# Kernel optimization log

Hardware: AMD Instinct MI355X
Metric: run time of the kernel (lower is better)

Reference implementation:

```python
import jax, jax.numpy as jnp
import numpy as np

N = 50000       # original graph nodes (= number of subgraphs, one per node)
S = 10          # nodes per subgraph
M = N * S       # combined subgraph nodes
E = 2_000_000   # combined subgraph edges
E0 = 1_000_000  # original edges
NIN, HOP, NOUT, L = 64, 16, 128, 3
D = NIN + HOP   # conv width (80)


def setup_inputs() -> dict:
    key = jax.random.key(0)
    ks = iter(jax.random.split(key, 40))
    rng = np.random.default_rng(0)

    # structured index tensors: subgraph b occupies rows [b*S, (b+1)*S); row b*S is the centroid
    sub_batch = np.repeat(np.arange(N, dtype=np.int64), S)
    nodes_mapper = rng.integers(0, N, size=M, dtype=np.int64)
    nodes_mapper[::S] = np.arange(N)           # centroid: mapper == batch id
    hop_indicator = rng.integers(1, 5, size=M).astype(np.int64)
    hop_indicator[::S] = 0                     # centroid is hop 0
    edge_index = rng.integers(0, M, size=(2, E), dtype=np.int64)
    edges_mapper = rng.integers(0, E0, size=E, dtype=np.int64)

    def lin(k, fin, fout):
        return jax.random.normal(k, (fin, fout), jnp.float32) / np.sqrt(fin)

    inp = dict(
        x=jax.random.normal(next(ks), (N, NIN), jnp.float32),
        edge_attr=jax.random.normal(next(ks), (E0, D), jnp.float32),
        hop_table=jax.random.normal(next(ks), (20, HOP), jnp.float32),
        conv_W=jax.random.normal(next(ks), (L, D, D), jnp.float32) / np.sqrt(D),
        bn_g=jnp.ones((L, D), jnp.float32),
        bn_b=jnp.zeros((L, D), jnp.float32),
        oe_W0=lin(next(ks), D, NOUT), oe_b0=jnp.zeros((NOUT,), jnp.float32),
        oe_W1=lin(next(ks), NOUT, NOUT), oe_b1=jnp.zeros((NOUT,), jnp.float32),
        oe_W2=lin(next(ks), NOUT, NOUT), oe_b2=jnp.zeros((NOUT,), jnp.float32),
        st_W0=lin(next(ks), NOUT, NOUT), st_b0=jnp.zeros((NOUT,), jnp.float32),
        st_W1=lin(next(ks), NOUT, NOUT), st_b1=jnp.zeros((NOUT,), jnp.float32),
        st_W2=lin(next(ks), NOUT, NOUT), st_b2=jnp.zeros((NOUT,), jnp.float32),
        ct_W0=lin(next(ks), NOUT, NOUT), ct_b0=jnp.zeros((NOUT,), jnp.float32),
        ct_W1=lin(next(ks), NOUT, NOUT), ct_b1=jnp.zeros((NOUT,), jnp.float32),
        ct_W2=lin(next(ks), NOUT, NOUT), ct_b2=jnp.zeros((NOUT,), jnp.float32),
        gc_W=lin(next(ks), HOP, NOUT), gc_b=jnp.zeros((NOUT,), jnp.float32),
        gs_W=lin(next(ks), HOP, NOUT), gs_b=jnp.zeros((NOUT,), jnp.float32),
        gx_W=lin(next(ks), HOP, NOUT), gx_b=jnp.zeros((NOUT,), jnp.float32),
        nodes_mapper=jnp.asarray(nodes_mapper),
        edge_index=jnp.asarray(edge_index),
        edges_mapper=jnp.asarray(edges_mapper),
        sub_batch=jnp.asarray(sub_batch),
        hop_indicator=jnp.asarray(hop_indicator),
    )
    return inp


def _mlp3(h, W0, b0, W1, b1, W2, b2, final_act):
    h = jax.nn.relu(h @ W0 + b0)
    h = jax.nn.relu(h @ W1 + b1)
    h = h @ W2 + b2
    return jax.nn.relu(h) if final_act else h


def reference(x, edge_attr, hop_table, conv_W, bn_g, bn_b,
              oe_W0, oe_b0, oe_W1, oe_b1, oe_W2, oe_b2,
              st_W0, st_b0, st_W1, st_b1, st_W2, st_b2,
              ct_W0, ct_b0, ct_W1, ct_b1, ct_W2, ct_b2,
              gc_W, gc_b, gs_W, gs_b, gx_W, gx_b,
              nodes_mapper, edge_index, edges_mapper, sub_batch, hop_indicator):
    src, dst = edge_index[0], edge_index[1]
    ea = edge_attr[edges_mapper]                              # [E, D] gather
    hemb = hop_table[hop_indicator + 1]                       # [M, HOP]
    h = jnp.concatenate([x[nodes_mapper], hemb], axis=-1)     # [M, D]

    # GNN: nlayer x (GINE-style conv -> relu -> batchnorm(batch stats) -> residual)
    for l in range(L):
        msg = h[src] + ea                                     # [E, D]
        agg = jax.ops.segment_sum(msg, dst, num_segments=M)   # scatter-add
        h2 = jax.nn.relu(agg @ conv_W[l])
        mu = jnp.mean(h2, axis=0)
        var = jnp.var(h2, axis=0)
        h2 = (h2 - mu) * jax.lax.rsqrt(var + 1e-5) * bn_g[l] + bn_b[l]
        h = h2 + h                                            # residual

    # output encoder MLP (no final activation)
    h = _mlp3(h, oe_W0, oe_b0, oe_W1, oe_b1, oe_W2, oe_b2, False)  # [M, NOUT]

    # three views with sigmoid hop gates
    g_c = jax.nn.sigmoid(hemb @ gc_W + gc_b)
    g_s = jax.nn.sigmoid(hemb @ gs_W + gs_b)
    g_x = jax.nn.sigmoid(hemb @ gx_W + gx_b)

    cm = (nodes_mapper == sub_batch)[:, None]                 # centroid mask (one per subgraph)
    centroid_x = jax.ops.segment_sum(jnp.where(cm, h * g_c, 0.0), sub_batch, num_segments=N)
    subgraph_x = jax.ops.segment_sum(
        _mlp3(h, st_W0, st_b0, st_W1, st_b1, st_W2, st_b2, True) * g_s, sub_batch, num_segments=N)
    context_x = jax.ops.segment_sum(
        _mlp3(h, ct_W0, ct_b0, ct_W1, ct_b1, ct_W2, ct_b2, True) * g_x, nodes_mapper, num_segments=N)

    return centroid_x + subgraph_x + context_x                # embs_combine_mode='add'
```

## Files before the change

kernel.cpp:

```cpp
#include <hip/hip_runtime.h>


typedef __attribute__((ext_vector_type(8))) short bf16x8;
typedef __attribute__((ext_vector_type(4))) float f32x4;

static constexpr int cN = 50000;
static constexpr int cM = 500000;
static constexpr int cE = 2000000;
static constexpr int cTiles = cM / 16;

static constexpr size_t PCONV0 = 0, PCONV1 = 7680, PCONV2 = 15360, POE0 = 23040,
                        POE1 = 35328, POE2 = 51712, PST0 = 68096, PST1 = 84480,
                        PST2 = 100864, PCT0 = 117248, PCT1 = 133632, PCT2 = 150016;
static constexpr size_t PACK_BYTES = 166400 * 2 + 256;

__device__ __forceinline__ float b2f(unsigned short u) {
  union { unsigned int u; float f; } v; v.u = ((unsigned int)u) << 16; return v.f;
}
__device__ __forceinline__ unsigned short f2b(float f) {
  union { float f; unsigned int u; } v; v.f = f;
  unsigned int x = v.u;
  x += 0x7fffu + ((x >> 16) & 1u);
  return (unsigned short)(x >> 16);
}
__device__ __forceinline__ float sigm(float x) { return 1.0f / (1.0f + __expf(-x)); }
__device__ __forceinline__ f32x4 mfma16(bf16x8 a, bf16x8 b, f32x4 c) {
  return __builtin_amdgcn_mfma_f32_16x16x32_bf16(a, b, c, 0, 0, 0);
}

struct RepackDesc { const float* src; unsigned short* dst; int K; int N; int tiles; };
struct RepackArgs { RepackDesc d[12]; };

__global__ __launch_bounds__(256) void repack_kernel(RepackArgs a) {
  RepackDesc dd = a.d[blockIdx.y];
  int tile = blockIdx.x;
  if (tile >= dd.tiles) return;
  int ncb = dd.N >> 4;
  int c = tile / ncb, cb = tile - c * ncb;
  for (int e = threadIdx.x; e < 512; e += 256) {
    int lane = e >> 3, j = e & 7;
    int k = 32 * c + 8 * (lane >> 4) + j;
    int n = 16 * cb + (lane & 15);
    unsigned short v = (k < dd.K) ? f2b(dd.src[(size_t)k * dd.N + n]) : (unsigned short)0;
    dd.dst[(size_t)tile * 512 + e] = v;
  }
}

__global__ __launch_bounds__(256) void gate_build_kernel(
    const float* __restrict__ ht,
    const float* __restrict__ gsW, const float* __restrict__ gsb,
    const float* __restrict__ gcW, const float* __restrict__ gcb,
    const float* __restrict__ gxW, const float* __restrict__ gxb,
    float* __restrict__ gtab)
{
  int i = blockIdx.x * 256 + threadIdx.x;
  if (i >= 3 * 20 * 128) return;
  int g = i / 2560, rem = i - g * 2560;
  int hi = rem >> 7, col = rem & 127;
  const float* W  = (g == 0) ? gsW : (g == 1) ? gcW : gxW;
  const float* bb = (g == 0) ? gsb : (g == 1) ? gcb : gxb;
  float acc = bb[col];
  #pragma unroll
  for (int k = 0; k < 16; ++k) acc += ht[hi * 16 + k] * W[k * 128 + col];
  gtab[i] = sigm(acc);
}

__global__ __launch_bounds__(256) void build_h_kernel(
    const float* __restrict__ x, const float* __restrict__ ht,
    const int* __restrict__ nmap, const int* __restrict__ hop,
    unsigned short* __restrict__ h)
{
  int i = blockIdx.x * 256 + threadIdx.x;
  if (i >= cM * 20) return;
  int row = i / 20, cc = i - row * 20;
  int col = cc * 4;
  float4 f;
  if (col < 64) {
    f = *(const float4*)(x + (size_t)nmap[row] * 64 + col);
  } else {
    int hi = hop[row] + 1;
    f = *(const float4*)(ht + (size_t)hi * 16 + (col - 64));
  }
  ushort4 o; o.x = f2b(f.x); o.y = f2b(f.y); o.z = f2b(f.z); o.w = f2b(f.w);
  *(ushort4*)(h + (size_t)row * 80 + col) = o;
}

__global__ __launch_bounds__(256) void hist_kernel(const int* __restrict__ ei, int* __restrict__ deg) {
  int e = blockIdx.x * 256 + threadIdx.x;
  if (e < cE) atomicAdd(&deg[ei[cE + e]], 1);
}

__global__ __launch_bounds__(256) void scan1_kernel(const int* __restrict__ deg, int* __restrict__ bsum) {
  __shared__ int s[256];
  int i = blockIdx.x * 256 + threadIdx.x;
  s[threadIdx.x] = (i < cM) ? deg[i] : 0;
  __syncthreads();
  for (int o = 128; o > 0; o >>= 1) {
    if (threadIdx.x < o) s[threadIdx.x] += s[threadIdx.x + o];
    __syncthreads();
  }
  if (threadIdx.x == 0) bsum[blockIdx.x] = s[0];
}

__global__ void scan2_kernel(int* __restrict__ bsum, int nb) {
  if (threadIdx.x == 0 && blockIdx.x == 0) {
    int acc = 0;
    for (int i = 0; i < nb; ++i) { int t = bsum[i]; bsum[i] = acc; acc += t; }
  }
}

__global__ __launch_bounds__(256) void scan3_kernel(
    const int* __restrict__ deg, const int* __restrict__ bsum,
    int* __restrict__ rowptr, int* __restrict__ cursor)
{
  __shared__ int s[256];
  int i = blockIdx.x * 256 + threadIdx.x;
  int v = (i < cM) ? deg[i] : 0;
  s[threadIdx.x] = v;
  __syncthreads();
  for (int o = 1; o < 256; o <<= 1) {
    int t = (threadIdx.x >= o) ? s[threadIdx.x - o] : 0;
    __syncthreads();
    s[threadIdx.x] += t;
    __syncthreads();
  }
  if (i < cM) {
    int ex = bsum[blockIdx.x] + s[threadIdx.x] - v;
    rowptr[i] = ex; cursor[i] = ex;
  }
  if (i == cM - 1) rowptr[cM] = bsum[blockIdx.x] + s[threadIdx.x];
}

__global__ __launch_bounds__(256) void scatter_kernel(
    const int* __restrict__ ei, const int* __restrict__ emap,
    int* __restrict__ cursor, int* __restrict__ srcs, int* __restrict__ em2)
{
  int e = blockIdx.x * 256 + threadIdx.x;
  if (e >= cE) return;
  int d = ei[cE + e];
  int pos = atomicAdd(&cursor[d], 1);
  srcs[pos] = ei[e];
  em2[pos] = emap[e];
}

__global__ __launch_bounds__(320) void eag_rowsum_kernel(
    const float* __restrict__ ea, const int* __restrict__ em2,
    const int* __restrict__ rowptr, unsigned short* __restrict__ eag)
{
  int t = threadIdx.x;
  int r = blockIdx.x * 16 + t / 20;
  int c = (t % 20) * 4;
  if (r >= cM) return;
  int p0 = rowptr[r], p1 = rowptr[r + 1];
  float4 acc = {0.f, 0.f, 0.f, 0.f};
  for (int p = p0; p < p1; ++p) {
    int em = em2[p];
    float4 v = *(const float4*)(ea + (size_t)em * 80 + c);
    acc.x += v.x; acc.y += v.y; acc.z += v.z; acc.w += v.w;
  }
  ushort4 o = {f2b(acc.x), f2b(acc.y), f2b(acc.z), f2b(acc.w)};
  *(ushort4*)(eag + (size_t)r * 80 + c) = o;
}

__global__ __launch_bounds__(320) void aggregate_kernel(
    const unsigned short* __restrict__ h, const unsigned short* __restrict__ eag,
    const int* __restrict__ rowptr, const int* __restrict__ srcs,
    unsigned short* __restrict__ Bo)
{
  int t = threadIdx.x;
  int r = blockIdx.x * 16 + t / 20;
  int c = (t % 20) * 4;
  if (r >= cM) return;
  int p0 = rowptr[r], p1 = rowptr[r + 1];
  ushort4 a0 = *(const ushort4*)(eag + (size_t)r * 80 + c);
  float4 acc = {b2f(a0.x), b2f(a0.y), b2f(a0.z), b2f(a0.w)};
  for (int p = p0; p < p1; ++p) {
    int s = srcs[p];
    ushort4 v = *(const ushort4*)(h + (size_t)s * 80 + c);
    acc.x += b2f(v.x); acc.y += b2f(v.y); acc.z += b2f(v.z); acc.w += b2f(v.w);
  }
  ushort4 o = {f2b(acc.x), f2b(acc.y), f2b(acc.z), f2b(acc.w)};
  *(ushort4*)(Bo + (size_t)r * 80 + c) = o;
}

__global__ __launch_bounds__(256) void edge_scatter_kernel(
    const unsigned short* __restrict__ h, const float* __restrict__ ea,
    const int* __restrict__ ei, const int* __restrict__ emap,
    float* __restrict__ agg)
{
  int i = blockIdx.x * 256 + threadIdx.x;
  if (i >= cE * 20) return;
  int e = i / 20, q = i - e * 20;
  int src = ei[e], dst = ei[cE + e], em = emap[e];
  ushort4 hv = *(const ushort4*)(h + (size_t)src * 80 + q * 4);
  float4 ev = *(const float4*)(ea + (size_t)em * 80 + q * 4);
  float* ap = agg + (size_t)dst * 80 + q * 4;
  atomicAdd(ap + 0, b2f(hv.x) + ev.x);
  atomicAdd(ap + 1, b2f(hv.y) + ev.y);
  atomicAdd(ap + 2, b2f(hv.z) + ev.z);
  atomicAdd(ap + 3, b2f(hv.w) + ev.w);
}

template<bool F32IO>
__global__ __launch_bounds__(256) void conv_gemm_kernel(
    void* __restrict__ aggv, const unsigned short* __restrict__ Bp)
{
  __shared__ __align__(16) unsigned short Bl[7680];
  #pragma unroll
  for (int i = threadIdx.x; i < 960; i += 256)
    ((uint4*)Bl)[i] = ((const uint4*)Bp)[i];
  __syncthreads();
  int lane = threadIdx.x & 63, wave = threadIdx.x >> 6;
  int tile0 = (blockIdx.x * 4 + wave) * 4;
  int quad = lane >> 4, m = lane & 15;

  bf16x8 a[4][3];
  #pragma unroll
  for (int tt = 0; tt < 4; ++tt) {
    int tile = tile0 + tt;
    bool act = tile < cTiles;
    size_t rowA = (size_t)tile * 16 + m;
    #pragma unroll
    for (int c = 0; c < 3; ++c) {
      bf16x8 av = {0, 0, 0, 0, 0, 0, 0, 0};
      int k = 32 * c + 8 * quad;
      if (act && k + 8 <= 80) {
        if constexpr (F32IO) {
          const float* p = (const float*)aggv + rowA * 80 + k;
          float4 f0 = *(const float4*)p;
          float4 f1 = *(const float4*)(p + 4);
          av[0] = (short)f2b(f0.x); av[1] = (short)f2b(f0.y);
          av[2] = (short)f2b(f0.z); av[3] = (short)f2b(f0.w);
          av[4] = (short)f2b(f1.x); av[5] = (short)f2b(f1.y);
          av[6] = (short)f2b(f1.z); av[7] = (short)f2b(f1.w);
        } else {
          av = *(const bf16x8*)((const unsigned short*)aggv + rowA * 80 + k);
        }
      }
      a[tt][c] = av;
    }
  }

  #pragma unroll
  for (int tt = 0; tt < 4; ++tt) {
    int tile = tile0 + tt;
    bool act = tile < cTiles;
    #pragma unroll
    for (int cb = 0; cb < 5; ++cb) {
      f32x4 acc = {0.f, 0.f, 0.f, 0.f};
      #pragma unroll
      for (int c = 0; c < 3; ++c)
        acc = mfma16(a[tt][c], *(const bf16x8*)(Bl + ((size_t)(c * 5 + cb) * 64 + lane) * 8), acc);
      int col = cb * 16 + m;
      #pragma unroll
      for (int i2 = 0; i2 < 4; ++i2) {
        size_t row = (size_t)tile * 16 + quad * 4 + i2;
        if (act) {
          float v = fmaxf(acc[i2], 0.0f);
          if constexpr (F32IO) ((float*)aggv)[row * 80 + col] = v;
          else ((unsigned short*)aggv)[row * 80 + col] = f2b(v);
        }
      }
    }
  }
}

template<bool F32IO>
__global__ __launch_bounds__(256) void stats_kernel(
    const void* __restrict__ h2v, float* __restrict__ stats)
{
  __shared__ __align__(16) float ssum[12 * 80];
  __shared__ __align__(16) float ssq[12 * 80];
  int t = threadIdx.x;
  int cc = t % 20, slot = t / 20;
  if (slot < 12) {
    float s0 = 0, s1 = 0, s2 = 0, s3 = 0, q0 = 0, q1 = 0, q2 = 0, q3 = 0;
    for (int row = blockIdx.x * 12 + slot; row < cM; row += gridDim.x * 12) {
      float f0, f1, f2, f3;
      if constexpr (F32IO) {
        float4 v = *(const float4*)((const float*)h2v + (size_t)row * 80 + cc * 4);
        f0 = v.x; f1 = v.y; f2 = v.z; f3 = v.w;
      } else {
        ushort4 v = *(const ushort4*)((const unsigned short*)h2v + (size_t)row * 80 + cc * 4);
        f0 = b2f(v.x); f1 = b2f(v.y); f2 = b2f(v.z); f3 = b2f(v.w);
      }
      s0 += f0; s1 += f1; s2 += f2; s3 += f3;
      q0 += f0 * f0; q1 += f1 * f1; q2 += f2 * f2; q3 += f3 * f3;
    }
    int base = slot * 80 + cc * 4;
    ssum[base + 0] = s0; ssum[base + 1] = s1; ssum[base + 2] = s2; ssum[base + 3] = s3;
    ssq[base + 0] = q0; ssq[base + 1] = q1; ssq[base + 2] = q2; ssq[base + 3] = q3;
  }
  __syncthreads();
  if (t < 20) {
    for (int j = 0; j < 4; ++j) {
      int c = t * 4 + j;
      float s = 0, q = 0;
      for (int sl = 0; sl < 12; ++sl) { s += ssum[sl * 80 + c]; q += ssq[sl * 80 + c]; }
      atomicAdd(&stats[c], s);
      atomicAdd(&stats[80 + c], q);
    }
  }
}

template<bool F32IO>
__global__ __launch_bounds__(256) void bn_residual_kernel(
    const void* __restrict__ h2v, const float* __restrict__ stats,
    const float* __restrict__ g, const float* __restrict__ b,
    unsigned short* __restrict__ h)
{
  int i = blockIdx.x * 256 + threadIdx.x;
  if (i >= cM * 20) return;
  int row = i / 20, cc = i - row * 20;
  int col = cc * 4;
  float in2[4];
  if constexpr (F32IO) {
    float4 v2 = *(const float4*)((const float*)h2v + (size_t)row * 80 + col);
    in2[0] = v2.x; in2[1] = v2.y; in2[2] = v2.z; in2[3] = v2.w;
  } else {
    ushort4 v2 = *(const ushort4*)((const unsigned short*)h2v + (size_t)row * 80 + col);
    in2[0] = b2f(v2.x); in2[1] = b2f(v2.y); in2[2] = b2f(v2.z); in2[3] = b2f(v2.w);
  }
  ushort4 vh = *(const ushort4*)(h + (size_t)row * 80 + col);
  const float invM = 1.0f / (float)cM;
  unsigned short inh[4] = {vh.x, vh.y, vh.z, vh.w};
  unsigned short o[4];
  #pragma unroll
  for (int j = 0; j < 4; ++j) {
    int c = col + j;
    float mu = stats[c] * invM;
    float var = fmaxf(stats[80 + c] * invM - mu * mu, 0.0f);
    float inv = rsqrtf(var + 1e-5f);
    float val = (in2[j] - mu) * inv * g[c] + b[c] + b2f(inh[j]);
    o[j] = f2b(val);
  }
  ushort4 ov = {o[0], o[1], o[2], o[3]};
  *(ushort4*)(h + (size_t)row * 80 + col) = ov;
}

__device__ __forceinline__ void tb_put(unsigned short* tbw, int row, int col, unsigned short v) {
  int g = (col >> 3) ^ (row & 7);
  tbw[row * 128 + (g << 3) + (col & 7)] = v;
}

__device__ __forceinline__ void tb_to_a(bf16x8* a, const unsigned short* tbw, int lane) {
  int quad = lane >> 4, m = lane & 15;
  #pragma unroll
  for (int c = 0; c < 4; ++c) {
    int sg = ((c << 2) | quad) ^ (m & 7);
    a[c] = *(const bf16x8*)(tbw + m * 128 + (sg << 3));
  }
}

template<int KCH>
__device__ __forceinline__ void layer_relu(
    const bf16x8* a, const unsigned short* Wl, const float* bl,
    unsigned short* tbw, int lane)
{
  int quad = lane >> 4, m = lane & 15;
  #pragma unroll
  for (int cb = 0; cb < 8; ++cb) {
    f32x4 acc = {0.f, 0.f, 0.f, 0.f};
    #pragma unroll
    for (int c = 0; c < KCH; ++c)
      acc = mfma16(a[c], *(const bf16x8*)(Wl + ((size_t)(c * 8 + cb) * 64 + lane) * 8), acc);
    int col = cb * 16 + m;
    float bv = bl[col];
    #pragma unroll
    for (int i2 = 0; i2 < 4; ++i2)
      tb_put(tbw, quad * 4 + i2, col, f2b(fmaxf(acc[i2] + bv, 0.0f)));
  }
}

__device__ __forceinline__ void stageW(unsigned short* Wbuf, const unsigned short* src, int nU4, int t) {
  const uint4* s = (const uint4*)src;
  uint4* d = (uint4*)Wbuf;
  for (int i = t; i < nU4; i += 256) d[i] = s[i];
}

__global__ __launch_bounds__(256, 3) void tail_fused_kernel(
    const unsigned short* __restrict__ h,
    const unsigned short* __restrict__ packs,
    const float* __restrict__ oeb0, const float* __restrict__ oeb1, const float* __restrict__ oeb2,
    const float* __restrict__ stb0, const float* __restrict__ stb1, const float* __restrict__ stb2,
    const float* __restrict__ ctb0, const float* __restrict__ ctb1, const float* __restrict__ ctb2,
    const float* __restrict__ gtab,
    const int* __restrict__ hop, const int* __restrict__ nmap, const int* __restrict__ sb,
    float* __restrict__ outp)
{
  __shared__ __align__(16) unsigned short Wbuf[16384];
  __shared__ __align__(16) unsigned short tb[4][2048];
  __shared__ __align__(16) float biasl[9][128];

  int t = threadIdx.x;
  stageW(Wbuf, packs + POE0, 1536, t);
  if (t < 128) {
    biasl[0][t] = oeb0[t]; biasl[1][t] = oeb1[t]; biasl[2][t] = oeb2[t];
    biasl[3][t] = stb0[t]; biasl[4][t] = stb1[t]; biasl[5][t] = stb2[t];
    biasl[6][t] = ctb0[t]; biasl[7][t] = ctb1[t]; biasl[8][t] = ctb2[t];
  }
  __syncthreads();

  int lane = t & 63, wave = t >> 6;
  int tile = blockIdx.x * 4 + wave;
  bool act = tile < cTiles;
  int quad = lane >> 4, m = lane & 15;
  size_t rowA = (size_t)tile * 16 + m;

  bf16x8 aw[4];
  #pragma unroll
  for (int c = 0; c < 4; ++c) {
    bf16x8 av = {0, 0, 0, 0, 0, 0, 0, 0};
    int k = 32 * c + 8 * quad;
    if (act && c < 3 && k + 8 <= 80)
      av = *(const bf16x8*)(h + rowA * 80 + k);
    aw[c] = av;
  }

  layer_relu<3>(aw, Wbuf, biasl[0], tb[wave], lane);
  tb_to_a(aw, tb[wave], lane);
  __syncthreads();
  stageW(Wbuf, packs + POE1, 2048, t);
  __syncthreads();
  layer_relu<4>(aw, Wbuf, biasl[1], tb[wave], lane);
  tb_to_a(aw, tb[wave], lane);
  __syncthreads();
  stageW(Wbuf, packs + POE2, 2048, t);
  __syncthreads();

  float o_out[8][4];
  bf16x8 a_oe[4];
  {
    #pragma unroll
    for (int cb = 0; cb < 8; ++cb) {
      f32x4 acc = {0.f, 0.f, 0.f, 0.f};
      #pragma unroll
      for (int c = 0; c < 4; ++c)
        acc = mfma16(aw[c], *(const bf16x8*)(Wbuf + ((size_t)(c * 8 + cb) * 64 + lane) * 8), acc);
      int col = cb * 16 + m;
      float bv = biasl[2][col];
      #pragma unroll
      for (int i2 = 0; i2 < 4; ++i2) {
        float val = acc[i2] + bv;
        o_out[cb][i2] = val;
        tb_put(tb[wave], quad * 4 + i2, col, f2b(val));
      }
    }
    tb_to_a(a_oe, tb[wave], lane);
  }
  __syncthreads();
  stageW(Wbuf, packs + PST0, 2048, t);
  __syncthreads();

  layer_relu<4>(a_oe, Wbuf, biasl[3], tb[wave], lane);
  tb_to_a(aw, tb[wave], lane);
  __syncthreads();
  stageW(Wbuf, packs + PST1, 2048, t);
  __syncthreads();
  layer_relu<4>(aw, Wbuf, biasl[4], tb[wave], lane);
  tb_to_a(aw, tb[wave], lane);
  __syncthreads();
  stageW(Wbuf, packs + PST2, 2048, t);
  float* red = (float*)&tb[0][0];
  for (int i = t; i < 1024; i += 256) red[i] = 0.0f;
  int sbBase = sb[blockIdx.x * 64];
  __syncthreads();

  int hi2[4], sbr[4], dstm[4]; bool mk[4];
  #pragma unroll
  for (int i2 = 0; i2 < 4; ++i2) {
    int row = tile * 16 + quad * 4 + i2;
    sbr[i2]  = act ? sb[row] : 0;
    dstm[i2] = act ? nmap[row] : 0;
    mk[i2]   = act && (dstm[i2] == sbr[i2]);
    hi2[i2]  = act ? (hop[row] + 1) : 0;
  }

  #pragma unroll
  for (int cb = 0; cb < 8; ++cb) {
    f32x4 acc = {0.f, 0.f, 0.f, 0.f};
    #pragma unroll
    for (int c = 0; c < 4; ++c)
      acc = mfma16(aw[c], *(const bf16x8*)(Wbuf + ((size_t)(c * 8 + cb) * 64 + lane) * 8), acc);
    int col = cb * 16 + m;
    float bv = biasl[5][col];
    #pragma unroll
    for (int i2 = 0; i2 < 4; ++i2) {
      float v = fmaxf(acc[i2] + bv, 0.0f) * gtab[hi2[i2] * 128 + col];
      if (mk[i2]) v += o_out[cb][i2] * gtab[2560 + hi2[i2] * 128 + col];
      if (act) {
        int slot = sbr[i2] - sbBase;
        if ((unsigned)slot < 8u) atomicAdd(&red[slot * 128 + col], v);
        else atomicAdd(outp + (size_t)sbr[i2] * 128 + col, v);
      }
    }
  }
  __syncthreads();
  for (int i = t; i < 1024; i += 256) {
    float v = red[i];
    if (v != 0.0f)
      atomicAdd(outp + (size_t)(sbBase + (i >> 7)) * 128 + (i & 127), v);
  }
  __syncthreads();
  stageW(Wbuf, packs + PCT0, 2048, t);
  __syncthreads();

  layer_relu<4>(a_oe, Wbuf, biasl[6], tb[wave], lane);
  tb_to_a(aw, tb[wave], lane);
  __syncthreads();
  stageW(Wbuf, packs + PCT1, 2048, t);
  __syncthreads();
  layer_relu<4>(aw, Wbuf, biasl[7], tb[wave], lane);
  tb_to_a(aw, tb[wave], lane);
  __syncthreads();
  stageW(Wbuf, packs + PCT2, 2048, t);
  __syncthreads();

  #pragma unroll
  for (int cb = 0; cb < 8; ++cb) {
    f32x4 acc = {0.f, 0.f, 0.f, 0.f};
    #pragma unroll
    for (int c = 0; c < 4; ++c)
      acc = mfma16(aw[c], *(const bf16x8*)(Wbuf + ((size_t)(c * 8 + cb) * 64 + lane) * 8), acc);
    int col = cb * 16 + m;
    float bv = biasl[8][col];
    #pragma unroll
    for (int i2 = 0; i2 < 4; ++i2) {
      float v = fmaxf(acc[i2] + bv, 0.0f) * gtab[5120 + hi2[i2] * 128 + col];
      if (act) atomicAdd(outp + (size_t)dstm[i2] * 128 + col, v);
    }
  }
}

extern "C" void kernel_launch(void* const* d_in, const int* in_sizes, int n_in,
                              void* d_out, int out_size, void* d_ws, size_t ws_size,
                              hipStream_t stream)
{
  const float* x     = (const float*)d_in[0];
  const float* eattr = (const float*)d_in[1];
  const float* htab  = (const float*)d_in[2];
  const float* convW = (const float*)d_in[3];
  const float* bng   = (const float*)d_in[4];
  const float* bnb   = (const float*)d_in[5];
  const float* oeW0 = (const float*)d_in[6];  const float* oeb0 = (const float*)d_in[7];
  const float* oeW1 = (const float*)d_in[8];  const float* oeb1 = (const float*)d_in[9];
  const float* oeW2 = (const float*)d_in[10]; const float* oeb2 = (const float*)d_in[11];
  const float* stW0 = (const float*)d_in[12]; const float* stb0 = (const float*)d_in[13];
  const float* stW1 = (const float*)d_in[14]; const float* stb1 = (const float*)d_in[15];
  const float* stW2 = (const float*)d_in[16]; const float* stb2 = (const float*)d_in[17];
  const float* ctW0 = (const float*)d_in[18]; const float* ctb0 = (const float*)d_in[19];
  const float* ctW1 = (const float*)d_in[20]; const float* ctb1 = (const float*)d_in[21];
  const float* ctW2 = (const float*)d_in[22]; const float* ctb2 = (const float*)d_in[23];
  const float* gcW = (const float*)d_in[24]; const float* gcb = (const float*)d_in[25];
  const float* gsW = (const float*)d_in[26]; const float* gsb = (const float*)d_in[27];
  const float* gxW = (const float*)d_in[28]; const float* gxb = (const float*)d_in[29];
  const int* nmap = (const int*)d_in[30];
  const int* ei   = (const int*)d_in[31];
  const int* emap = (const int*)d_in[32];
  const int* sb   = (const int*)d_in[33];
  const int* hop  = (const int*)d_in[34];

  if (n_in < 35 ||
      in_sizes[0] != cN * 64 || in_sizes[1] != 1000000 * 80 ||
      in_sizes[2] != 20 * 16 || in_sizes[3] != 3 * 80 * 80 ||
      in_sizes[30] != cM || in_sizes[31] != 2 * cE || in_sizes[32] != cE ||
      in_sizes[33] != cM || in_sizes[34] != cM || out_size != cN * 128)
    return;

  char* ws = (char*)d_ws;
  size_t off = 0;
  auto alloc = [&](size_t bytes) -> void* {
    void* p = ws + off; off += (bytes + 255) & ~(size_t)255; return p;
  };

  unsigned short* h    = (unsigned short*)alloc((size_t)cM * 80 * 2);
  unsigned short* Aeag = (unsigned short*)alloc((size_t)cM * 80 * 2);
  unsigned short* Bagg = (unsigned short*)alloc((size_t)cM * 80 * 2);
  int*   rowptr = (int*)alloc((size_t)(cM + 1) * 4);
  int*   srcs   = (int*)alloc((size_t)cE * 4);
  float* stats  = (float*)alloc(1024);
  float* gtab   = (float*)alloc(3 * 20 * 128 * 4);
  unsigned short* packs = (unsigned short*)alloc(PACK_BYTES);
  size_t needFast = off;
  bool fast = (ws_size >= needFast);

  float* aggF = nullptr;
  if (!fast) {
    off = 0;
    h     = (unsigned short*)alloc((size_t)cM * 80 * 2);
    aggF  = (float*)alloc((size_t)cM * 80 * 4);
    stats = (float*)alloc(1024);
    gtab  = (float*)alloc(3 * 20 * 128 * 4);
    packs = (unsigned short*)alloc(PACK_BYTES);
    if (ws_size < off) return;
  }

  RepackArgs ra;
  auto setd = [&](int idx, const float* src, size_t dstOff, int K, int Nn, int tiles) {
    ra.d[idx].src = src; ra.d[idx].dst = packs + dstOff;
    ra.d[idx].K = K; ra.d[idx].N = Nn; ra.d[idx].tiles = tiles;
  };
  setd(0, convW,          PCONV0, 80, 80, 15);
  setd(1, convW + 6400,   PCONV1, 80, 80, 15);
  setd(2, convW + 12800,  PCONV2, 80, 80, 15);
  setd(3, oeW0, POE0, 80, 128, 24);
  setd(4, oeW1, POE1, 128, 128, 32);
  setd(5, oeW2, POE2, 128, 128, 32);
  setd(6, stW0, PST0, 128, 128, 32);
  setd(7, stW1, PST1, 128, 128, 32);
  setd(8, stW2, PST2, 128, 128, 32);
  setd(9, ctW0, PCT0, 128, 128, 32);
  setd(10, ctW1, PCT1, 128, 128, 32);
  setd(11, ctW2, PCT2, 128, 128, 32);
  repack_kernel<<<dim3(32, 12), 256, 0, stream>>>(ra);
  gate_build_kernel<<<30, 256, 0, stream>>>(htab, gsW, gsb, gcW, gcb, gxW, gxb, gtab);

  const int elemBlocksM = (cM * 20 + 255) / 256;
  const int convBlocks  = (cTiles + 15) / 16;
  const int tailBlocks  = (cTiles + 3) / 4;
  const int rowBlocks   = (cM + 15) / 16;
  const int edgeB256    = (cE + 255) / 256;
  const int scanBlocks  = (cM + 255) / 256;

  build_h_kernel<<<elemBlocksM, 256, 0, stream>>>(x, htab, nmap, hop, h);
  hipMemsetAsync(d_out, 0, (size_t)cN * 128 * 4, stream);

  if (fast) {
    int* deg    = (int*)Bagg;
    int* cursor = deg + cM;
    int* em2    = cursor + cM;
    int* bsum   = em2 + cE;

    hipMemsetAsync(deg, 0, (size_t)cM * 4, stream);
    hist_kernel<<<edgeB256, 256, 0, stream>>>(ei, deg);
    scan1_kernel<<<scanBlocks, 256, 0, stream>>>(deg, bsum);
    scan2_kernel<<<1, 64, 0, stream>>>(bsum, scanBlocks);
    scan3_kernel<<<scanBlocks, 256, 0, stream>>>(deg, bsum, rowptr, cursor);
    scatter_kernel<<<edgeB256, 256, 0, stream>>>(ei, emap, cursor, srcs, em2);
    eag_rowsum_kernel<<<rowBlocks, 320, 0, stream>>>(eattr, em2, rowptr, Aeag);

    for (int l = 0; l < 3; ++l) {
      aggregate_kernel<<<rowBlocks, 320, 0, stream>>>(h, Aeag, rowptr, srcs, Bagg);
      conv_gemm_kernel<false><<<convBlocks, 256, 0, stream>>>(
          Bagg, packs + (l == 0 ? PCONV0 : l == 1 ? PCONV1 : PCONV2));
      hipMemsetAsync(stats, 0, 160 * 4, stream);
      stats_kernel<false><<<1024, 256, 0, stream>>>(Bagg, stats);
      bn_residual_kernel<false><<<elemBlocksM, 256, 0, stream>>>(
          Bagg, stats, bng + l * 80, bnb + l * 80, h);
    }
  } else {
    const int edgeBlocks = (cE * 20) / 256;
    for (int l = 0; l < 3; ++l) {
      hipMemsetAsync(aggF, 0, (size_t)cM * 80 * 4, stream);
      edge_scatter_kernel<<<edgeBlocks, 256, 0, stream>>>(h, eattr, ei, emap, aggF);
      conv_gemm_kernel<true><<<convBlocks, 256, 0, stream>>>(
          aggF, packs + (l == 0 ? PCONV0 : l == 1 ? PCONV1 : PCONV2));
      hipMemsetAsync(stats, 0, 160 * 4, stream);
      stats_kernel<true><<<1024, 256, 0, stream>>>(aggF, stats);
      bn_residual_kernel<true><<<elemBlocksM, 256, 0, stream>>>(
          aggF, stats, bng + l * 80, bnb + l * 80, h);
    }
  }

  tail_fused_kernel<<<tailBlocks, 256, 0, stream>>>(
      h, packs,
      oeb0, oeb1, oeb2, stb0, stb1, stb2, ctb0, ctb1, ctb2,
      gtab, hop, nmap, sb, (float*)d_out);
}
```

Measured before the change: 2.823 ms.

## Fuse aggregation with conv GEMM and prefetch tail MLP weights into registers

Merges the CSR gather-aggregate kernel with the conv GEMM. Each block aggregates 80 rows into shared memory, then runs MFMA on them with the conv weights staged in LDS, which removes one write and one read of the aggregate buffer per layer. In the tail kernel, the next layer's weights are loaded into registers during the current layer's compute and committed to LDS afterwards, replacing synchronous staging. The costs are more register pressure in the tail kernel and extra LDS in the fused kernel, which may lower occupancy.

Result: slower. 3.149 ms (+11.6%).

```diff
diff --git a/kernel.cpp b/kernel.cpp
--- a/kernel.cpp
+++ b/kernel.cpp
@@ -162,25 +162,62 @@
   *(ushort4*)(eag + (size_t)r * 80 + c) = o;
 }
 
-__global__ __launch_bounds__(320) void aggregate_kernel(
+__global__ __launch_bounds__(320) void agg_conv_kernel(
     const unsigned short* __restrict__ h, const unsigned short* __restrict__ eag,
     const int* __restrict__ rowptr, const int* __restrict__ srcs,
-    unsigned short* __restrict__ Bo)
-{
+    const unsigned short* __restrict__ Bp, unsigned short* __restrict__ h2)
+{
+  __shared__ __align__(16) unsigned short Bl[7680];
+  __shared__ __align__(16) unsigned short At[80 * 88];
   int t = threadIdx.x;
-  int r = blockIdx.x * 16 + t / 20;
+  for (int i = t; i < 960; i += 320) ((uint4*)Bl)[i] = ((const uint4*)Bp)[i];
+
+  int rloc = t / 20;
   int c = (t % 20) * 4;
-  if (r >= cM) return;
-  int p0 = rowptr[r], p1 = rowptr[r + 1];
-  ushort4 a0 = *(const ushort4*)(eag + (size_t)r * 80 + c);
-  float4 acc = {b2f(a0.x), b2f(a0.y), b2f(a0.z), b2f(a0.w)};
-  for (int p = p0; p < p1; ++p) {
-    int s = srcs[p];
-    ushort4 v = *(const ushort4*)(h + (size_t)s * 80 + c);
-    acc.x += b2f(v.x); acc.y += b2f(v.y); acc.z += b2f(v.z); acc.w += b2f(v.w);
-  }
-  ushort4 o = {f2b(acc.x), f2b(acc.y), f2b(acc.z), f2b(acc.w)};
-  *(ushort4*)(Bo + (size_t)r * 80 + c) = o;
+  int rowBase = blockIdx.x * 80;
+  #pragma unroll
+  for (int tt = 0; tt < 5; ++tt) {
+    int rl = tt * 16 + rloc;
+    int r = rowBase + rl;
+    ushort4 a0 = *(const ushort4*)(eag + (size_t)r * 80 + c);
+    float4 acc = {b2f(a0.x), b2f(a0.y), b2f(a0.z), b2f(a0.w)};
+    int p0 = rowptr[r], p1 = rowptr[r + 1];
+    for (int p = p0; p < p1; ++p) {
+      int s = srcs[p];
+      ushort4 v = *(const ushort4*)(h + (size_t)s * 80 + c);
+      acc.x += b2f(v.x); acc.y += b2f(v.y); acc.z += b2f(v.z); acc.w += b2f(v.w);
+    }
+    ushort4 o = {f2b(acc.x), f2b(acc.y), f2b(acc.z), f2b(acc.w)};
+    *(ushort4*)(At + (size_t)rl * 88 + c) = o;
+  }
+  __syncthreads();
+
+  int lane = t & 63, wave = t >> 6;
+  int quad = lane >> 4, m = lane & 15;
+  int rl0 = wave * 16;
+  size_t gr0 = (size_t)rowBase + rl0;
+
+  bf16x8 a[3];
+  #pragma unroll
+  for (int cc2 = 0; cc2 < 3; ++cc2) {
+    int k = 32 * cc2 + 8 * quad;
+    bf16x8 av = {0, 0, 0, 0, 0, 0, 0, 0};
+    if (k + 8 <= 80) av = *(const bf16x8*)(At + (size_t)(rl0 + m) * 88 + k);
+    a[cc2] = av;
+  }
+  #pragma unroll
+  for (int cb = 0; cb < 5; ++cb) {
+    f32x4 acc = {0.f, 0.f, 0.f, 0.f};
+    #pragma unroll
+    for (int cc2 = 0; cc2 < 3; ++cc2)
+      acc = mfma16(a[cc2], *(const bf16x8*)(Bl + ((size_t)(cc2 * 5 + cb) * 64 + lane) * 8), acc);
+    int col = cb * 16 + m;
+    #pragma unroll
+    for (int i2 = 0; i2 < 4; ++i2) {
+      size_t row = gr0 + quad * 4 + i2;
+      h2[row * 80 + col] = f2b(fmaxf(acc[i2], 0.0f));
+    }
+  }
 }
 
 __global__ __launch_bounds__(256) void edge_scatter_kernel(
@@ -393,14 +430,6 @@
   __shared__ __align__(16) float biasl[9][128];
 
   int t = threadIdx.x;
-  stageW(Wbuf, packs + POE0, 1536, t);
-  if (t < 128) {
-    biasl[0][t] = oeb0[t]; biasl[1][t] = oeb1[t]; biasl[2][t] = oeb2[t];
-    biasl[3][t] = stb0[t]; biasl[4][t] = stb1[t]; biasl[5][t] = stb2[t];
-    biasl[6][t] = ctb0[t]; biasl[7][t] = ctb1[t]; biasl[8][t] = ctb2[t];
-  }
-  __syncthreads();
-
   int lane = t & 63, wave = t >> 6;
   int tile = blockIdx.x * 4 + wave;
   bool act = tile < cTiles;
@@ -417,15 +446,36 @@
     aw[c] = av;
   }
 
+  stageW(Wbuf, packs + POE0, 1536, t);
+  if (t < 128) {
+    biasl[0][t] = oeb0[t]; biasl[1][t] = oeb1[t]; biasl[2][t] = oeb2[t];
+    biasl[3][t] = stb0[t]; biasl[4][t] = stb1[t]; biasl[5][t] = stb2[t];
+    biasl[6][t] = ctb0[t]; biasl[7][t] = ctb1[t]; biasl[8][t] = ctb2[t];
+  }
+  __syncthreads();
+
+  uint4 wreg[8];
+  auto preload = [&](size_t off) {
+    const uint4* s = (const uint4*)(packs + off);
+    #pragma unroll
+    for (int i = 0; i < 8; ++i) wreg[i] = s[t + i * 256];
+  };
+  auto commit = [&]() {
+    uint4* d = (uint4*)Wbuf;
+    #pragma unroll
+    for (int i = 0; i < 8; ++i) d[t + i * 256] = wreg[i];
+  };
+
+  preload(POE1);
   layer_relu<3>(aw, Wbuf, biasl[0], tb[wave], lane);
   tb_to_a(aw, tb[wave], lane);
   __syncthreads();
-  stageW(Wbuf, packs + POE1, 2048, t);
+  commit(); preload(POE2);
   __syncthreads();
   layer_relu<4>(aw, Wbuf, biasl[1], tb[wave], lane);
   tb_to_a(aw, tb[wave], lane);
   __syncthreads();
-  stageW(Wbuf, packs + POE2, 2048, t);
+  commit(); preload(PST0);
   __syncthreads();
 
   float o_out[8][4];
@@ -449,18 +499,18 @@
     tb_to_a(a_oe, tb[wave], lane);
   }
   __syncthreads();
-  stageW(Wbuf, packs + PST0, 2048, t);
+  commit(); preload(PST1);
   __syncthreads();
 
   layer_relu<4>(a_oe, Wbuf, biasl[3], tb[wave], lane);
   tb_to_a(aw, tb[wave], lane);
   __syncthreads();
-  stageW(Wbuf, packs + PST1, 2048, t);
+  commit(); preload(PST2);
   __syncthreads();
   layer_relu<4>(aw, Wbuf, biasl[4], tb[wave], lane);
   tb_to_a(aw, tb[wave], lane);
   __syncthreads();
-  stageW(Wbuf, packs + PST2, 2048, t);
+  commit(); preload(PCT0);
   float* red = (float*)&tb[0][0];
   for (int i = t; i < 1024; i += 256) red[i] = 0.0f;
   int sbBase = sb[blockIdx.x * 64];
@@ -496,24 +546,23 @@
     }
   }
   __syncthreads();
+  commit(); preload(PCT1);
   for (int i = t; i < 1024; i += 256) {
     float v = red[i];
     if (v != 0.0f)
       atomicAdd(outp + (size_t)(sbBase + (i >> 7)) * 128 + (i & 127), v);
   }
   __syncthreads();
-  stageW(Wbuf, packs + PCT0, 2048, t);
-  __syncthreads();
 
   layer_relu<4>(a_oe, Wbuf, biasl[6], tb[wave], lane);
   tb_to_a(aw, tb[wave], lane);
   __syncthreads();
-  stageW(Wbuf, packs + PCT1, 2048, t);
+  commit(); preload(PCT2);
   __syncthreads();
   layer_relu<4>(aw, Wbuf, biasl[7], tb[wave], lane);
   tb_to_a(aw, tb[wave], lane);
   __syncthreads();
-  stageW(Wbuf, packs + PCT2, 2048, t);
+  commit();
   __syncthreads();
 
   #pragma unroll
@@ -616,8 +665,9 @@
   gate_build_kernel<<<30, 256, 0, stream>>>(htab, gsW, gsb, gcW, gcb, gxW, gxb, gtab);
 
   const int elemBlocksM = (cM * 20 + 255) / 256;
+  const int tailBlocks  = (cTiles + 3) / 4;
+  const int aggcBlocks  = cM / 80;
   const int convBlocks  = (cTiles + 15) / 16;
-  const int tailBlocks  = (cTiles + 3) / 4;
   const int rowBlocks   = (cM + 15) / 16;
   const int edgeB256    = (cE + 255) / 256;
   const int scanBlocks  = (cM + 255) / 256;
@@ -640,9 +690,9 @@
     eag_rowsum_kernel<<<rowBlocks, 320, 0, stream>>>(eattr, em2, rowptr, Aeag);
 
     for (int l = 0; l < 3; ++l) {
-      aggregate_kernel<<<rowBlocks, 320, 0, stream>>>(h, Aeag, rowptr, srcs, Bagg);
-      conv_gemm_kernel<false><<<convBlocks, 256, 0, stream>>>(
-          Bagg, packs + (l == 0 ? PCONV0 : l == 1 ? PCONV1 : PCONV2));
+      agg_conv_kernel<<<aggcBlocks, 320, 0, stream>>>(
+          h, Aeag, rowptr, srcs,
+          packs + (l == 0 ? PCONV0 : l == 1 ? PCONV1 : PCONV2), Bagg);
       hipMemsetAsync(stats, 0, 160 * 4, stream);
       stats_kernel<false><<<1024, 256, 0, stream>>>(Bagg, stats);
       bn_residual_kernel<false><<<elemBlocksM, 256, 0, stream>>>(
```

## Fuse conv GEMM with BN stats and stage CSR indices in LDS

Applied to the files above, without the earlier changes.

Adds a conv_stats kernel that runs the conv GEMM with ReLU, writes bf16 output, and accumulates per-column sum and sum-of-squares through shared-memory atomics then global atomics. This removes the separate stats pass over the aggregated buffer in each of the three layers. The row-gather aggregate and eag kernels now load each block's edge index span into LDS cooperatively before gathering, instead of each thread reading indices from global memory. Risks are atomic contention on the 160 stats floats and LDS fallback overhead when a block's span exceeds 1024.

Result: faster. 2.518 ms (-10.8%).

```diff
diff --git a/kernel.cpp b/kernel.cpp
--- a/kernel.cpp
+++ b/kernel.cpp
@@ -147,16 +147,36 @@
     const float* __restrict__ ea, const int* __restrict__ em2,
     const int* __restrict__ rowptr, unsigned short* __restrict__ eag)
 {
+  __shared__ int s_idx[1024];
+  __shared__ int s_rp[17];
   int t = threadIdx.x;
-  int r = blockIdx.x * 16 + t / 20;
+  int rowBase = blockIdx.x * 16;
+  if (t <= 16) s_rp[t] = rowptr[rowBase + t];
+  __syncthreads();
+  int p0b = s_rp[0];
+  int span = s_rp[16] - p0b;
+  bool lds_ok = (span <= 1024);
+  if (lds_ok)
+    for (int i = t; i < span; i += 320) s_idx[i] = em2[p0b + i];
+  __syncthreads();
+
+  int rl = t / 20;
+  int r = rowBase + rl;
   int c = (t % 20) * 4;
-  if (r >= cM) return;
-  int p0 = rowptr[r], p1 = rowptr[r + 1];
+  int p0 = s_rp[rl], p1 = s_rp[rl + 1];
   float4 acc = {0.f, 0.f, 0.f, 0.f};
-  for (int p = p0; p < p1; ++p) {
-    int em = em2[p];
-    float4 v = *(const float4*)(ea + (size_t)em * 80 + c);
-    acc.x += v.x; acc.y += v.y; acc.z += v.z; acc.w += v.w;
+  if (lds_ok) {
+    for (int p = p0; p < p1; ++p) {
+      int em = s_idx[p - p0b];
+      float4 v = *(const float4*)(ea + (size_t)em * 80 + c);
+      acc.x += v.x; acc.y += v.y; acc.z += v.z; acc.w += v.w;
+    }
+  } else {
+    for (int p = p0; p < p1; ++p) {
+      int em = em2[p];
+      float4 v = *(const float4*)(ea + (size_t)em * 80 + c);
+      acc.x += v.x; acc.y += v.y; acc.z += v.z; acc.w += v.w;
+    }
   }
   ushort4 o = {f2b(acc.x), f2b(acc.y), f2b(acc.z), f2b(acc.w)};
   *(ushort4*)(eag + (size_t)r * 80 + c) = o;
@@ -167,17 +187,37 @@
     const int* __restrict__ rowptr, const int* __restrict__ srcs,
     unsigned short* __restrict__ Bo)
 {
+  __shared__ int s_idx[1024];
+  __shared__ int s_rp[17];
   int t = threadIdx.x;
-  int r = blockIdx.x * 16 + t / 20;
+  int rowBase = blockIdx.x * 16;
+  if (t <= 16) s_rp[t] = rowptr[rowBase + t];
+  __syncthreads();
+  int p0b = s_rp[0];
+  int span = s_rp[16] - p0b;
+  bool lds_ok = (span <= 1024);
+  if (lds_ok)
+    for (int i = t; i < span; i += 320) s_idx[i] = srcs[p0b + i];
+  __syncthreads();
+
+  int rl = t / 20;
+  int r = rowBase + rl;
   int c = (t % 20) * 4;
-  if (r >= cM) return;
-  int p0 = rowptr[r], p1 = rowptr[r + 1];
+  int p0 = s_rp[rl], p1 = s_rp[rl + 1];
   ushort4 a0 = *(const ushort4*)(eag + (size_t)r * 80 + c);
   float4 acc = {b2f(a0.x), b2f(a0.y), b2f(a0.z), b2f(a0.w)};
-  for (int p = p0; p < p1; ++p) {
-    int s = srcs[p];
-    ushort4 v = *(const ushort4*)(h + (size_t)s * 80 + c);
-    acc.x += b2f(v.x); acc.y += b2f(v.y); acc.z += b2f(v.z); acc.w += b2f(v.w);
+  if (lds_ok) {
+    for (int p = p0; p < p1; ++p) {
+      int s = s_idx[p - p0b];
+      ushort4 v = *(const ushort4*)(h + (size_t)s * 80 + c);
+      acc.x += b2f(v.x); acc.y += b2f(v.y); acc.z += b2f(v.z); acc.w += b2f(v.w);
+    }
+  } else {
+    for (int p = p0; p < p1; ++p) {
+      int s = srcs[p];
+      ushort4 v = *(const ushort4*)(h + (size_t)s * 80 + c);
+      acc.x += b2f(v.x); acc.y += b2f(v.y); acc.z += b2f(v.z); acc.w += b2f(v.w);
+    }
   }
   ushort4 o = {f2b(acc.x), f2b(acc.y), f2b(acc.z), f2b(acc.w)};
   *(ushort4*)(Bo + (size_t)r * 80 + c) = o;
@@ -199,6 +239,72 @@
   atomicAdd(ap + 1, b2f(hv.y) + ev.y);
   atomicAdd(ap + 2, b2f(hv.z) + ev.z);
   atomicAdd(ap + 3, b2f(hv.w) + ev.w);
+}
+
+__global__ __launch_bounds__(256) void conv_stats_kernel(
+    unsigned short* __restrict__ agg, const unsigned short* __restrict__ Bp,
+    float* __restrict__ stats)
+{
+  __shared__ __align__(16) unsigned short Bl[7680];
+  __shared__ float s_red[160];
+  int t = threadIdx.x;
+  #pragma unroll
+  for (int i = t; i < 960; i += 256)
+    ((uint4*)Bl)[i] = ((const uint4*)Bp)[i];
+  if (t < 160) s_red[t] = 0.0f;
+  __syncthreads();
+  int lane = t & 63, wave = t >> 6;
+  int tile0 = (blockIdx.x * 4 + wave) * 4;
+  int quad = lane >> 4, m = lane & 15;
+
+  bf16x8 a[4][3];
+  #pragma unroll
+  for (int tt = 0; tt < 4; ++tt) {
+    int tile = tile0 + tt;
+    bool act = tile < cTiles;
+    size_t rowA = (size_t)tile * 16 + m;
+    #pragma unroll
+    for (int c = 0; c < 3; ++c) {
+      bf16x8 av = {0, 0, 0, 0, 0, 0, 0, 0};
+      int k = 32 * c + 8 * quad;
+      if (act && k + 8 <= 80)
+        av = *(const bf16x8*)(agg + rowA * 80 + k);
+      a[tt][c] = av;
+    }
+  }
+
+  float lsum[5] = {0, 0, 0, 0, 0}, lsq[5] = {0, 0, 0, 0, 0};
+  #pragma unroll
+  for (int tt = 0; tt < 4; ++tt) {
+    int tile = tile0 + tt;
+    bool act = tile < cTiles;
+    #pragma unroll
+    for (int cb = 0; cb < 5; ++cb) {
+      f32x4 acc = {0.f, 0.f, 0.f, 0.f};
+      #pragma unroll
+      for (int c = 0; c < 3; ++c)
+        acc = mfma16(a[tt][c], *(const bf16x8*)(Bl + ((size_t)(c * 5 + cb) * 64 + lane) * 8), acc);
+      int col = cb * 16 + m;
+      #pragma unroll
+      for (int i2 = 0; i2 < 4; ++i2) {
+        if (act) {
+          float v = fmaxf(acc[i2], 0.0f);
+          size_t row = (size_t)tile * 16 + quad * 4 + i2;
+          agg[row * 80 + col] = f2b(v);
+          lsum[cb] += v;
+          lsq[cb]  += v * v;
+        }
+      }
+    }
+  }
+  #pragma unroll
+  for (int cb = 0; cb < 5; ++cb) {
+    int col = cb * 16 + m;
+    atomicAdd(&s_red[col], lsum[cb]);
+    atomicAdd(&s_red[80 + col], lsq[cb]);
+  }
+  __syncthreads();
+  if (t < 160) atomicAdd(&stats[t], s_red[t]);
 }
 
 template<bool F32IO>
@@ -616,8 +722,8 @@
   gate_build_kernel<<<30, 256, 0, stream>>>(htab, gsW, gsb, gcW, gcb, gxW, gxb, gtab);
 
   const int elemBlocksM = (cM * 20 + 255) / 256;
+  const int tailBlocks  = (cTiles + 3) / 4;
   const int convBlocks  = (cTiles + 15) / 16;
-  const int tailBlocks  = (cTiles + 3) / 4;
   const int rowBlocks   = (cM + 15) / 16;
   const int edgeB256    = (cE + 255) / 256;
   const int scanBlocks  = (cM + 255) / 256;
@@ -641,10 +747,9 @@
 
     for (int l = 0; l < 3; ++l) {
       aggregate_kernel<<<rowBlocks, 320, 0, stream>>>(h, Aeag, rowptr, srcs, Bagg);
-      conv_gemm_kernel<false><<<convBlocks, 256, 0, stream>>>(
-          Bagg, packs + (l == 0 ? PCONV0 : l == 1 ? PCONV1 : PCONV2));
       hipMemsetAsync(stats, 0, 160 * 4, stream);
-      stats_kernel<false><<<1024, 256, 0, stream>>>(Bagg, stats);
+      conv_stats_kernel<<<convBlocks, 256, 0, stream>>>(
+          Bagg, packs + (l == 0 ? PCONV0 : l == 1 ? PCONV1 : PCONV2), stats);
       bn_residual_kernel<false><<<elemBlocksM, 256, 0, stream>>>(
           Bagg, stats, bng + l * 80, bnb + l * 80, h);
     }
```
